# Performance work log

Hardware: AMD Instinct MI355X
Metric: run time of the kernel (lower is better)

Reference implementation:

```python
import jax, jax.numpy as jnp
import numpy as np

DIM, DEPTH, HEADS, DIM_HEAD, MLP = 768, 6, 12, 64, 3072
INNER = HEADS * DIM_HEAD
B, N = 8, 1024
SCALE = DIM_HEAD ** -0.5
EPS = 1e-5


def _ln(x, g, b):
    m = jnp.mean(x, -1, keepdims=True)
    v = jnp.mean(jnp.square(x - m), -1, keepdims=True)
    return (x - m) * jax.lax.rsqrt(v + EPS) * g + b


def _ternary(w):
    # BitNet-style ternary quant with straight-through estimator
    s = jnp.mean(jnp.abs(w)) + 1e-8
    wq = jnp.clip(jnp.round(w / s), -1.0, 1.0) * s
    return w + jax.lax.stop_gradient(wq - w)


def setup_inputs() -> dict:
    key = jax.random.key(0)
    ks = jax.random.split(key, 8)
    d = {
        'x': jax.random.normal(ks[0], (B, N, DIM), jnp.float32),
        'ln1_g': jnp.ones((DEPTH, DIM), jnp.float32),
        'ln1_b': jnp.zeros((DEPTH, DIM), jnp.float32),
        'Wqkv': jax.random.normal(ks[1], (DEPTH, 3 * INNER, DIM), jnp.float32) * 0.02,
        'ln2_g': jnp.ones((DEPTH, INNER), jnp.float32),
        'ln2_b': jnp.zeros((DEPTH, INNER), jnp.float32),
        'Wo': jax.random.normal(ks[2], (DEPTH, DIM, INNER), jnp.float32) * 0.02,
        'bo': jnp.zeros((DEPTH, DIM), jnp.float32),
        'ffln1_g': jnp.ones((DEPTH, DIM), jnp.float32),
        'ffln1_b': jnp.zeros((DEPTH, DIM), jnp.float32),
        'W1': jax.random.normal(ks[3], (DEPTH, MLP, DIM), jnp.float32) * 0.02,
        'b1': jnp.zeros((DEPTH, MLP), jnp.float32),
        'ffln2_g': jnp.ones((DEPTH, MLP), jnp.float32),
        'ffln2_b': jnp.zeros((DEPTH, MLP), jnp.float32),
        'W2': jax.random.normal(ks[4], (DEPTH, DIM, MLP), jnp.float32) * 0.02,
        'b2': jnp.zeros((DEPTH, DIM), jnp.float32),
    }
    return d


def _forward(x, ln1_g, ln1_b, Wqkv, ln2_g, ln2_b, Wo, bo,
             ffln1_g, ffln1_b, W1, b1, ffln2_g, ffln2_b, W2, b2):
    depth = Wqkv.shape[0]
    # layers 0..depth-2 ternary, last layer plain linear
    flag = jnp.concatenate([jnp.ones((depth - 1,), x.dtype), jnp.zeros((1,), x.dtype)])

    def block(h, p):
        (g1, b1n, wqkv, g2, b2n, wo, bo_, fg1, fb1, w1, bb1, fg2, fb2, w2, bb2, f) = p

        def mt(w):
            return f * _ternary(w) + (1.0 - f) * w

        y = _ln(h, g1, b1n)
        qkv = jnp.einsum('bnd,ed->bne', y, mt(wqkv))  # [B,N,3*INNER]
        q, k, v = jnp.split(qkv, 3, axis=-1)
        def heads(t):
            return t.reshape(B, N, HEADS, DIM_HEAD).transpose(0, 2, 1, 3)
        q, k, v = heads(q), heads(k), heads(v)
        attn = jax.nn.softmax(jnp.einsum('bhnd,bhmd->bhnm', q, k) * SCALE, axis=-1)
        o = jnp.einsum('bhnm,bhmd->bhnd', attn, v)
        o = o.transpose(0, 2, 1, 3).reshape(B, N, INNER)
        o = _ln(o, g2, b2n)
        o = jnp.einsum('bne,de->bnd', o, mt(wo)) + bo_
        h = h + o
        y = _ln(h, fg1, fb1)
        y = jnp.einsum('bnd,md->bnm', y, mt(w1)) + bb1
        y = jax.nn.gelu(y, approximate=False)
        y = _ln(y, fg2, fb2)
        y = jnp.einsum('bnm,dm->bnd', y, mt(w2)) + bb2
        return h + y, None

    xs = (ln1_g, ln1_b, Wqkv, ln2_g, ln2_b, Wo, bo,
          ffln1_g, ffln1_b, W1, b1, ffln2_g, ffln2_b, W2, b2, flag)
    out, _ = jax.lax.scan(block, x, xs)
    return out


def reference(x, ln1_g, ln1_b, Wqkv, ln2_g, ln2_b, Wo, bo,
              ffln1_g, ffln1_b, W1, b1, ffln2_g, ffln2_b, W2, b2):
    return _forward(x, ln1_g, ln1_b, Wqkv, ln2_g, ln2_b, Wo, bo,
                    ffln1_g, ffln1_b, W1, b1, ffln2_g, ffln2_b, W2, b2)
```

## Files before the change

kernel.cpp:

```cpp
#include <hip/hip_runtime.h>
#include <hip/hip_bf16.h>
#include <math.h>

typedef __bf16 bf16_t;
typedef __bf16 bf16x4 __attribute__((ext_vector_type(4)));
typedef __bf16 bf16x8 __attribute__((ext_vector_type(8)));
typedef float  f32x4  __attribute__((ext_vector_type(4)));

#define TOKENS 8192
#define DIMV   768
#define INNERV 768
#define QKVW   2304
#define MLPW   3072
#define NSEQ   1024
#define NB     8
#define NH     12
#define DH     64

enum { EP_STORE = 0, EP_BIAS_RES = 1, EP_BIAS_GELU = 2 };

__device__ __forceinline__ void gload_lds16(const bf16_t* g, bf16_t* l)
{
  __builtin_amdgcn_global_load_lds((const __attribute__((address_space(1))) void*)g,
                                   (__attribute__((address_space(3))) void*)l,
                                   16, 0, 0);
}

__device__ __forceinline__ float gelu_fast(float x)
{
  const float z = fabsf(x) * 0.70710678118654752f;
  const float d = fmaf(0.3275911f, z, 1.0f);
  const float t = 1.0f / d;
  float p = fmaf(t, 1.061405429f, -1.453152027f);
  p = fmaf(t, p, 1.421413741f);
  p = fmaf(t, p, -0.284496736f);
  p = fmaf(t, p, 0.254829592f);
  p = t * p;
  const float e = __expf(-z * z);
  float erfv = fmaf(-p, e, 1.0f);
  erfv = copysignf(erfv, x);
  return 0.5f * x * (1.0f + erfv);
}

template <int BM>
__global__ __launch_bounds__(256)
void gemm_nt(const bf16_t* __restrict__ A, const bf16_t* __restrict__ B,
             const int K, const int N, const int mode,
             const float* __restrict__ sacc_p, const float sinvn, const float sbias,
             const float* __restrict__ bias,
             float* __restrict__ resid,
             bf16_t* __restrict__ outb,
             float* __restrict__ fout)
{
  constexpr int MI = BM / 32;
  constexpr int WR = BM / 2;
  __shared__ __align__(16) bf16_t lsAll[3 * BM * 32 + 3 * 128 * 32];
  bf16_t* lsA = lsAll;
  bf16_t* lsB = lsAll + 3 * BM * 32;
  const int tid  = threadIdx.x;
  const int lane = tid & 63;
  const int wave = tid >> 6;
  const int wm = wave >> 1, wn = wave & 1;
  const int bm = blockIdx.x, bn = blockIdx.y;

  const int srB   = wave * 32 + (lane >> 2);
  const int fswB  = (srB >> 1) & 3;
  const int scolB = ((lane & 3) ^ fswB) * 8;
  const bf16_t* gB = B + (size_t)(bn * 128 + srB) * K + scolB;
  const int lb0 = srB * 32 + (lane & 3) * 8;
  const int lb1 = (srB + 16) * 32 + (lane & 3) * 8;

  const int srA   = (BM == 128) ? srB : (wave * 16 + (lane >> 2));
  const int fswA  = (srA >> 1) & 3;
  const int scolA = ((lane & 3) ^ fswA) * 8;
  const bf16_t* gA = A + (size_t)(bm * BM + srA) * K + scolA;
  const int la0 = srA * 32 + (lane & 3) * 8;
  const int la1 = (srA + 16) * 32 + (lane & 3) * 8;

  f32x4 acc[MI][4];
#pragma unroll
  for (int i = 0; i < MI; i++)
#pragma unroll
    for (int j = 0; j < 4; j++) acc[i][j] = (f32x4){0.f, 0.f, 0.f, 0.f};

  const int fr   = ((lane & 15) >> 1) & 3;
  const int rsl  = ((lane >> 4) ^ fr) * 8;
  const int arow = (wm * WR + (lane & 15)) * 32 + rsl;
  const int brow = (wn * 64 + (lane & 15)) * 32 + rsl;

  auto stage = [&](int b, int kb) {
    gload_lds16(gA + kb, &lsA[b * BM * 32 + la0]);
    if constexpr (BM == 128) gload_lds16(gA + (size_t)16 * K + kb, &lsA[b * BM * 32 + la1]);
    gload_lds16(gB + kb, &lsB[b * 128 * 32 + lb0]);
    gload_lds16(gB + (size_t)16 * K + kb, &lsB[b * 128 * 32 + lb1]);
  };
  auto compute = [&](int b) {
    bf16x8 af[MI], bfv[4];
#pragma unroll
    for (int i = 0; i < MI; i++) af[i]  = *(const bf16x8*)&lsA[b * BM * 32 + arow + i * 16 * 32];
#pragma unroll
    for (int j = 0; j < 4; j++)  bfv[j] = *(const bf16x8*)&lsB[b * 128 * 32 + brow + j * 16 * 32];
#pragma unroll
    for (int i = 0; i < MI; i++)
#pragma unroll
      for (int j = 0; j < 4; j++)
        acc[i][j] = __builtin_amdgcn_mfma_f32_16x16x32_bf16(af[i], bfv[j], acc[i][j], 0, 0, 0);
  };

  const int NT = K / 32;
  stage(0, 0);
  stage(1, 32);
  int cb = 0, sb = 2;
  for (int t = 0; t < NT - 1; ++t) {
    if constexpr (BM == 128) asm volatile("s_waitcnt vmcnt(4)" ::: "memory");
    else                     asm volatile("s_waitcnt vmcnt(3)" ::: "memory");
    __builtin_amdgcn_s_barrier();
    __builtin_amdgcn_sched_barrier(0);
    compute(cb);
    if (t + 2 < NT) stage(sb, (t + 2) * 32);
    cb = (cb == 2) ? 0 : cb + 1;
    sb = (sb == 2) ? 0 : sb + 1;
  }
  asm volatile("s_waitcnt vmcnt(0)" ::: "memory");
  __builtin_amdgcn_s_barrier();
  __builtin_amdgcn_sched_barrier(0);
  compute(cb);

  __syncthreads();
  const float s = (*sacc_p) * sinvn + sbias;
  const int lr0 = wm * WR + (lane >> 4) * 4;
  const int lc0 = wn * 64 + (lane & 15);

  if (mode == EP_BIAS_RES) {
    float* ep = (float*)lsAll;
#pragma unroll
    for (int i = 0; i < MI; i++)
#pragma unroll
      for (int j = 0; j < 4; j++) {
        const float bcol = bias[bn * 128 + lc0 + j * 16];
#pragma unroll
        for (int r = 0; r < 4; r++)
          ep[(lr0 + i * 16 + r) * 132 + lc0 + j * 16] = acc[i][j][r] * s + bcol;
      }
    __syncthreads();
#pragma unroll
    for (int it = 0; it < BM / 8; ++it) {
      const int lr = it * 8 + (tid >> 5);
      const int lc = (tid & 31) * 4;
      f32x4 v = *(const f32x4*)&ep[lr * 132 + lc];
      const size_t idx = (size_t)(bm * BM + lr) * N + bn * 128 + lc;
      f32x4 rv = *(const f32x4*)&resid[idx];
      if (fout) *(f32x4*)&fout[idx]  = rv + v;
      else      *(f32x4*)&resid[idx] = rv + v;
    }
  } else {
    bf16_t* ep = lsAll;
#pragma unroll
    for (int i = 0; i < MI; i++)
#pragma unroll
      for (int j = 0; j < 4; j++) {
        const int col = bn * 128 + lc0 + j * 16;
#pragma unroll
        for (int r = 0; r < 4; r++) {
          const float v = acc[i][j][r] * s;
          ep[(lr0 + i * 16 + r) * 136 + lc0 + j * 16] =
              (mode == EP_STORE) ? (bf16_t)v : (bf16_t)gelu_fast(v + bias[col]);
        }
      }
    __syncthreads();
#pragma unroll
    for (int it = 0; it < BM / 16; ++it) {
      const int lr = it * 16 + (tid >> 4);
      const int lc = (tid & 15) * 8;
      bf16x8 v = *(const bf16x8*)&ep[lr * 136 + lc];
      *(bf16x8*)&outb[(size_t)(bm * BM + lr) * N + bn * 128 + lc] = v;
    }
  }
}

template <typename TIN>
__global__ __launch_bounds__(256)
void ln_kern(const TIN* __restrict__ x, const float* __restrict__ g,
             const float* __restrict__ b, bf16_t* __restrict__ y, const int W)
{
  const int row = blockIdx.x;
  const int tid = threadIdx.x;
  const TIN* xr = x + (size_t)row * W;
  float s = 0.f, s2 = 0.f;
  if constexpr (sizeof(TIN) == 4) {
    const f32x4* xv = (const f32x4*)xr;
    for (int i = tid; i < W / 4; i += 256) {
      f32x4 v = xv[i];
#pragma unroll
      for (int e = 0; e < 4; e++) { s += v[e]; s2 += v[e] * v[e]; }
    }
  } else {
    const bf16x8* xv = (const bf16x8*)xr;
    for (int i = tid; i < W / 8; i += 256) {
      bf16x8 v = xv[i];
#pragma unroll
      for (int e = 0; e < 8; e++) { const float f = (float)v[e]; s += f; s2 += f * f; }
    }
  }
#pragma unroll
  for (int off = 32; off > 0; off >>= 1) {
    s  += __shfl_xor(s,  off, 64);
    s2 += __shfl_xor(s2, off, 64);
  }
  __shared__ float red[8];
  if ((tid & 63) == 0) { red[(tid >> 6) * 2] = s; red[(tid >> 6) * 2 + 1] = s2; }
  __syncthreads();
  const float ts  = red[0] + red[2] + red[4] + red[6];
  const float ts2 = red[1] + red[3] + red[5] + red[7];
  const float invW = 1.0f / (float)W;
  const float mean = ts * invW;
  const float var  = fmaxf(ts2 * invW - mean * mean, 0.f);
  const float rs   = rsqrtf(var + 1e-5f);
  bf16_t* yr = y + (size_t)row * W;
  const f32x4* gv = (const f32x4*)g;
  const f32x4* bv = (const f32x4*)b;
  if constexpr (sizeof(TIN) == 4) {
    const f32x4* xv = (const f32x4*)xr;
    bf16x4* yv = (bf16x4*)yr;
    for (int i = tid; i < W / 4; i += 256) {
      f32x4 v = xv[i], gg = gv[i], bb = bv[i];
      bf16x4 o;
#pragma unroll
      for (int e = 0; e < 4; e++) o[e] = (bf16_t)((v[e] - mean) * rs * gg[e] + bb[e]);
      yv[i] = o;
    }
  } else {
    const bf16x8* xv = (const bf16x8*)xr;
    bf16x8* yv = (bf16x8*)yr;
    for (int i = tid; i < W / 8; i += 256) {
      bf16x8 v = xv[i];
      f32x4 g0 = gv[2 * i], g1 = gv[2 * i + 1];
      f32x4 b0 = bv[2 * i], b1 = bv[2 * i + 1];
      bf16x8 o;
#pragma unroll
      for (int e = 0; e < 4; e++) o[e]     = (bf16_t)(((float)v[e]     - mean) * rs * g0[e] + b0[e]);
#pragma unroll
      for (int e = 0; e < 4; e++) o[e + 4] = (bf16_t)(((float)v[e + 4] - mean) * rs * g1[e] + b1[e]);
      yv[i] = o;
    }
  }
}

__global__ __launch_bounds__(256)
void attn_mfma(const bf16_t* __restrict__ qkv, bf16_t* __restrict__ o)
{
  __shared__ __align__(16) bf16_t Ks[64][72];
  __shared__ __align__(16) bf16_t Vt[64][72];
  __shared__ __align__(16) bf16_t Pw[4][16][72];
  const float SCL = 0.125f * 1.44269504088896f;
  const int tid  = threadIdx.x;
  const int lane = tid & 63;
  const int wave = tid >> 6;
  const int quad = lane >> 4;
  const int l15  = lane & 15;
  const int qb = blockIdx.x, hh = blockIdx.y, bb = blockIdx.z;
  const size_t tokbase = (size_t)bb * NSEQ;

  const int qrow = qb * 64 + wave * 16 + l15;
  bf16x8 qf[2];
  {
    const bf16_t* qp = qkv + (tokbase + qrow) * QKVW + hh * DH;
    qf[0] = *(const bf16x8*)(qp + quad * 8);
    qf[1] = *(const bf16x8*)(qp + 32 + quad * 8);
  }

  f32x4 Ot[4];
#pragma unroll
  for (int i = 0; i < 4; i++) Ot[i] = (f32x4){0.f, 0.f, 0.f, 0.f};
  float m2[4], lp[4];
#pragma unroll
  for (int r = 0; r < 4; r++) { m2[r] = -1e30f; lp[r] = 0.f; }

  const int skv = tid & 63;
  const int sd  = (tid >> 6) * 16;

  bf16x8 k0, k1, v0, v1;
  {
    const bf16_t* kp = qkv + (tokbase + skv) * QKVW + INNERV + hh * DH + sd;
    k0 = *(const bf16x8*)kp;
    k1 = *(const bf16x8*)(kp + 8);
    v0 = *(const bf16x8*)(kp + INNERV);
    v1 = *(const bf16x8*)(kp + INNERV + 8);
  }

  for (int kt = 0; kt < NSEQ / 64; ++kt) {
    __syncthreads();
    *(bf16x8*)&Ks[skv][sd]     = k0;
    *(bf16x8*)&Ks[skv][sd + 8] = k1;
#pragma unroll
    for (int e = 0; e < 8; e++) { Vt[sd + e][skv] = v0[e]; Vt[sd + 8 + e][skv] = v1[e]; }
    __syncthreads();

    bf16x8 nk0 = k0, nk1 = k1, nv0 = v0, nv1 = v1;
    if (kt + 1 < NSEQ / 64) {
      const bf16_t* kp = qkv + (tokbase + (kt + 1) * 64 + skv) * QKVW + INNERV + hh * DH + sd;
      nk0 = *(const bf16x8*)kp;
      nk1 = *(const bf16x8*)(kp + 8);
      nv0 = *(const bf16x8*)(kp + INNERV);
      nv1 = *(const bf16x8*)(kp + INNERV + 8);
    }

    f32x4 st[4];
    __builtin_amdgcn_s_setprio(1);
#pragma unroll
    for (int nt = 0; nt < 4; nt++) {
      bf16x8 b0 = *(const bf16x8*)&Ks[nt * 16 + l15][quad * 8];
      bf16x8 b1 = *(const bf16x8*)&Ks[nt * 16 + l15][32 + quad * 8];
      f32x4 c = (f32x4){0.f, 0.f, 0.f, 0.f};
      c = __builtin_amdgcn_mfma_f32_16x16x32_bf16(qf[0], b0, c, 0, 0, 0);
      c = __builtin_amdgcn_mfma_f32_16x16x32_bf16(qf[1], b1, c, 0, 0, 0);
      st[nt] = c;
    }
    __builtin_amdgcn_s_setprio(0);

    float lm[4];
#pragma unroll
    for (int r = 0; r < 4; r++)
      lm[r] = fmaxf(fmaxf(st[0][r], st[1][r]), fmaxf(st[2][r], st[3][r]));
    const bool ok = (lm[0] * SCL <= m2[0] + 8.f) && (lm[1] * SCL <= m2[1] + 8.f) &&
                    (lm[2] * SCL <= m2[2] + 8.f) && (lm[3] * SCL <= m2[3] + 8.f);
    if (!__all(ok)) {
#pragma unroll
      for (int r = 0; r < 4; r++) {
        float v = lm[r];
        v = fmaxf(v, __shfl_xor(v, 1, 64));
        v = fmaxf(v, __shfl_xor(v, 2, 64));
        v = fmaxf(v, __shfl_xor(v, 4, 64));
        v = fmaxf(v, __shfl_xor(v, 8, 64));
        const float rmax2 = v * SCL;
        const float mnew = fmaxf(m2[r], rmax2);
        const float alpha = exp2f(m2[r] - mnew);
        m2[r] = mnew;
        lp[r] *= alpha;
#pragma unroll
        for (int dt = 0; dt < 4; dt++) Ot[dt][r] *= alpha;
      }
    }
#pragma unroll
    for (int nt = 0; nt < 4; nt++) {
#pragma unroll
      for (int r = 0; r < 4; r++) {
        const float p = exp2f(fmaf(st[nt][r], SCL, -m2[r]));
        lp[r] += p;
        Pw[wave][quad * 4 + r][nt * 16 + l15] = (bf16_t)p;
      }
    }

    asm volatile("s_waitcnt lgkmcnt(0)" ::: "memory");
    __builtin_amdgcn_sched_barrier(0);

    __builtin_amdgcn_s_setprio(1);
#pragma unroll
    for (int kk = 0; kk < 2; kk++) {
      bf16x8 pa = *(const bf16x8*)&Pw[wave][l15][kk * 32 + quad * 8];
#pragma unroll
      for (int dt = 0; dt < 4; dt++) {
        bf16x8 vb = *(const bf16x8*)&Vt[dt * 16 + l15][kk * 32 + quad * 8];
        Ot[dt] = __builtin_amdgcn_mfma_f32_16x16x32_bf16(pa, vb, Ot[dt], 0, 0, 0);
      }
    }
    __builtin_amdgcn_s_setprio(0);

    k0 = nk0; k1 = nk1; v0 = nv0; v1 = nv1;
  }

  float inv[4];
#pragma unroll
  for (int r = 0; r < 4; r++) {
    float v = lp[r];
    v += __shfl_xor(v, 1, 64);
    v += __shfl_xor(v, 2, 64);
    v += __shfl_xor(v, 4, 64);
    v += __shfl_xor(v, 8, 64);
    inv[r] = 1.0f / v;
  }
#pragma unroll
  for (int dt = 0; dt < 4; dt++) {
#pragma unroll
    for (int r = 0; r < 4; r++) {
      const int q = qb * 64 + wave * 16 + quad * 4 + r;
      const int d = dt * 16 + l15;
      o[(tokbase + q) * INNERV + hh * DH + d] = (bf16_t)(Ot[dt][r] * inv[r]);
    }
  }
}

__global__ __launch_bounds__(64)
void zero_kern(float* __restrict__ p)
{
  p[threadIdx.x] = 0.f;
}

__global__ __launch_bounds__(256)
void absmean4_kern(const float* __restrict__ w0, const float* __restrict__ w1,
                   const float* __restrict__ w2, const float* __restrict__ w3,
                   const long n0, const long n1, const long n2, const long n3,
                   float* __restrict__ acc)
{
  const int t = blockIdx.y;
  const float* w = (t == 0) ? w0 : (t == 1) ? w1 : (t == 2) ? w2 : w3;
  const long  n  = (t == 0) ? n0 : (t == 1) ? n1 : (t == 2) ? n2 : n3;
  const int tid = threadIdx.x;
  float s = 0.f;
  const size_t stride = (size_t)256 * gridDim.x * 4;
  for (size_t i = ((size_t)blockIdx.x * 256 + tid) * 4; i < (size_t)n; i += stride) {
    f32x4 v = *(const f32x4*)(w + i);
    s += fabsf(v[0]) + fabsf(v[1]) + fabsf(v[2]) + fabsf(v[3]);
  }
#pragma unroll
  for (int off = 32; off > 0; off >>= 1) s += __shfl_xor(s, off, 64);
  __shared__ float red[4];
  if ((tid & 63) == 0) red[tid >> 6] = s;
  __syncthreads();
  if (tid == 0) atomicAdd(&acc[t], red[0] + red[1] + red[2] + red[3]);
}

__global__ __launch_bounds__(256)
void quant4_kern(const float* __restrict__ w0, const float* __restrict__ w1,
                 const float* __restrict__ w2, const float* __restrict__ w3,
                 bf16_t* __restrict__ q0, bf16_t* __restrict__ q1,
                 bf16_t* __restrict__ q2, bf16_t* __restrict__ q3,
                 const int n40, const int n41, const int n42, const int n43,
                 const float* __restrict__ acc,
                 const float inv0, const float inv1, const float inv2, const float inv3)
{
  const int t = blockIdx.y;
  const float* w = (t == 0) ? w0 : (t == 1) ? w1 : (t == 2) ? w2 : w3;
  bf16_t*      q = (t == 0) ? q0 : (t == 1) ? q1 : (t == 2) ? q2 : q3;
  const int   n4 = (t == 0) ? n40 : (t == 1) ? n41 : (t == 2) ? n42 : n43;
  const float iv = (t == 0) ? inv0 : (t == 1) ? inv1 : (t == 2) ? inv2 : inv3;
  const int i = blockIdx.x * 256 + threadIdx.x;
  if (i >= n4) return;
  const float s = acc[t] * iv + 1e-8f;
  f32x4 v = ((const f32x4*)w)[i];
  bf16x4 o;
#pragma unroll
  for (int e = 0; e < 4; e++) {
    float qv = rintf(v[e] / s);
    qv = fminf(1.f, fmaxf(-1.f, qv));
    o[e] = (bf16_t)qv;
  }
  ((bf16x4*)q)[i] = o;
}

__global__ __launch_bounds__(256)
void cast4_kern(const float* __restrict__ w0, const float* __restrict__ w1,
                const float* __restrict__ w2, const float* __restrict__ w3,
                bf16_t* __restrict__ q0, bf16_t* __restrict__ q1,
                bf16_t* __restrict__ q2, bf16_t* __restrict__ q3,
                const int n40, const int n41, const int n42, const int n43)
{
  const int t = blockIdx.y;
  const float* w = (t == 0) ? w0 : (t == 1) ? w1 : (t == 2) ? w2 : w3;
  bf16_t*      q = (t == 0) ? q0 : (t == 1) ? q1 : (t == 2) ? q2 : q3;
  const int   n4 = (t == 0) ? n40 : (t == 1) ? n41 : (t == 2) ? n42 : n43;
  const int i = blockIdx.x * 256 + threadIdx.x;
  if (i >= n4) return;
  f32x4 v = ((const f32x4*)w)[i];
  bf16x4 o;
#pragma unroll
  for (int e = 0; e < 4; e++) o[e] = (bf16_t)v[e];
  ((bf16x4*)q)[i] = o;
}

__global__ __launch_bounds__(256)
void copyf_kern(const float* __restrict__ in, float* __restrict__ out, const int n4)
{
  const int i = blockIdx.x * 256 + threadIdx.x;
  if (i < n4) ((f32x4*)out)[i] = ((const f32x4*)in)[i];
}

extern "C" void kernel_launch(void* const* d_in, const int* in_sizes, int n_in,
                              void* d_out, int out_size, void* d_ws, size_t ws_size,
                              hipStream_t stream)
{
  const float* x     = (const float*)d_in[0];
  const float* ln1_g = (const float*)d_in[1];
  const float* ln1_b = (const float*)d_in[2];
  const float* Wqkv  = (const float*)d_in[3];
  const float* ln2_g = (const float*)d_in[4];
  const float* ln2_b = (const float*)d_in[5];
  const float* Wo    = (const float*)d_in[6];
  const float* bo    = (const float*)d_in[7];
  const float* fg1   = (const float*)d_in[8];
  const float* fb1   = (const float*)d_in[9];
  const float* W1    = (const float*)d_in[10];
  const float* b1    = (const float*)d_in[11];
  const float* fg2   = (const float*)d_in[12];
  const float* fb2   = (const float*)d_in[13];
  const float* W2    = (const float*)d_in[14];
  const float* b2    = (const float*)d_in[15];

  char* ws = (char*)d_ws;
  size_t off = 0;
  float*  sacc  = (float*)(ws + off);  off += 256;
  float*  h     = (float*)(ws + off);  off += (size_t)TOKENS * DIMV * 4;
  bf16_t* bigA  = (bf16_t*)(ws + off); off += (size_t)TOKENS * MLPW * 2;
  bf16_t* bigB  = (bf16_t*)(ws + off); off += (size_t)TOKENS * MLPW * 2;
  bf16_t* q_qkv = (bf16_t*)(ws + off); off += (size_t)QKVW * DIMV * 2;
  bf16_t* q_o   = (bf16_t*)(ws + off); off += (size_t)DIMV * INNERV * 2;
  bf16_t* q_1   = (bf16_t*)(ws + off); off += (size_t)MLPW * DIMV * 2;
  bf16_t* q_2   = (bf16_t*)(ws + off); off += (size_t)DIMV * MLPW * 2;

  bf16_t* obuf   = bigA;
  bf16_t* ln2out = bigA + (size_t)TOKENS * INNERV;

  zero_kern<<<1, 64, 0, stream>>>(sacc);
  copyf_kern<<<TOKENS * DIMV / 4 / 256, 256, 0, stream>>>(x, h, TOKENS * DIMV / 4);

  for (int lyr = 0; lyr < 6; ++lyr) {
    const float* wqkv_l = Wqkv + (size_t)lyr * QKVW * DIMV;
    const float* wo_l   = Wo   + (size_t)lyr * DIMV * INNERV;
    const float* w1_l   = W1   + (size_t)lyr * MLPW * DIMV;
    const float* w2_l   = W2   + (size_t)lyr * DIMV * MLPW;
    const float *sq, *so, *s1, *s2p;
    float iq, io, i1, i2, bq, bo2, bb1v, bb2v;
    if (lyr < 5) {
      absmean4_kern<<<dim3(64, 4), 256, 0, stream>>>(
          wqkv_l, wo_l, w1_l, w2_l,
          (long)QKVW * DIMV, (long)DIMV * INNERV, (long)MLPW * DIMV, (long)DIMV * MLPW,
          &sacc[lyr * 4]);
      quant4_kern<<<dim3(MLPW * DIMV / 1024, 4), 256, 0, stream>>>(
          wqkv_l, wo_l, w1_l, w2_l, q_qkv, q_o, q_1, q_2,
          QKVW * DIMV / 4, DIMV * INNERV / 4, MLPW * DIMV / 4, DIMV * MLPW / 4,
          &sacc[lyr * 4],
          1.0f / (QKVW * DIMV), 1.0f / (DIMV * INNERV), 1.0f / (MLPW * DIMV), 1.0f / (DIMV * MLPW));
      sq = &sacc[lyr * 4 + 0]; iq = 1.0f / (QKVW * DIMV); bq = 1e-8f;
      so = &sacc[lyr * 4 + 1]; io = 1.0f / (DIMV * INNERV); bo2 = 1e-8f;
      s1 = &sacc[lyr * 4 + 2]; i1 = 1.0f / (MLPW * DIMV); bb1v = 1e-8f;
      s2p = &sacc[lyr * 4 + 3]; i2 = 1.0f / (DIMV * MLPW); bb2v = 1e-8f;
    } else {
      cast4_kern<<<dim3(MLPW * DIMV / 1024, 4), 256, 0, stream>>>(
          wqkv_l, wo_l, w1_l, w2_l, q_qkv, q_o, q_1, q_2,
          QKVW * DIMV / 4, DIMV * INNERV / 4, MLPW * DIMV / 4, DIMV * MLPW / 4);
      sq = so = s1 = s2p = &sacc[63];
      iq = io = i1 = i2 = 0.f;
      bq = bo2 = bb1v = bb2v = 1.0f;
    }

    ln_kern<float><<<TOKENS, 256, 0, stream>>>(h, ln1_g + lyr * DIMV, ln1_b + lyr * DIMV, bigA, DIMV);
    gemm_nt<128><<<dim3(64, QKVW / 128), 256, 0, stream>>>(bigA, q_qkv, DIMV, QKVW, EP_STORE, sq, iq, bq, nullptr, nullptr, bigB, nullptr);
    attn_mfma<<<dim3(NSEQ / 64, NH, NB), 256, 0, stream>>>(bigB, obuf);
    ln_kern<bf16_t><<<TOKENS, 256, 0, stream>>>(obuf, ln2_g + lyr * INNERV, ln2_b + lyr * INNERV, ln2out, INNERV);
    gemm_nt<64><<<dim3(TOKENS / 64, DIMV / 128), 256, 0, stream>>>(ln2out, q_o, INNERV, DIMV, EP_BIAS_RES, so, io, bo2, bo + lyr * DIMV, h, nullptr, nullptr);
    ln_kern<float><<<TOKENS, 256, 0, stream>>>(h, fg1 + lyr * DIMV, fb1 + lyr * DIMV, bigA, DIMV);
    gemm_nt<128><<<dim3(64, MLPW / 128), 256, 0, stream>>>(bigA, q_1, DIMV, MLPW, EP_BIAS_GELU, s1, i1, bb1v, b1 + lyr * MLPW, nullptr, bigB, nullptr);
    ln_kern<bf16_t><<<TOKENS, 256, 0, stream>>>(bigB, fg2 + lyr * MLPW, fb2 + lyr * MLPW, bigA, MLPW);
    gemm_nt<64><<<dim3(TOKENS / 64, DIMV / 128), 256, 0, stream>>>(bigA, q_2, MLPW, DIMV, EP_BIAS_RES, s2p, i2, bb2v, b2 + lyr * DIMV, h, nullptr,
                                                                   (lyr == 5) ? (float*)d_out : nullptr);
  }
}
```

Baseline: 2.210 ms.

## Double attention query tile to 128 rows with 512 threads and XCD-aware block order

Each attention block now uses 8 waves covering 128 query rows, so every K/V tile staged in shared memory serves twice as many queries. Per-thread staging load is halved to match. Block IDs are remapped so consecutive blocks spread across the 8 XCDs while blocks of the same head stay grouped for L2 reuse. The absmean reduction grid is also widened. The trade is fewer blocks in flight, and larger blocks may lower occupancy.

```diff
diff --git a/kernel.cpp b/kernel.cpp
--- a/kernel.cpp
+++ b/kernel.cpp
@@ -246,22 +246,28 @@
   }
 }
 
-__global__ __launch_bounds__(256)
+__global__ __launch_bounds__(512)
 void attn_mfma(const bf16_t* __restrict__ qkv, bf16_t* __restrict__ o)
 {
   __shared__ __align__(16) bf16_t Ks[64][72];
   __shared__ __align__(16) bf16_t Vt[64][72];
-  __shared__ __align__(16) bf16_t Pw[4][16][72];
+  __shared__ __align__(16) bf16_t Pw[8][16][72];
   const float SCL = 0.125f * 1.44269504088896f;
   const int tid  = threadIdx.x;
   const int lane = tid & 63;
   const int wave = tid >> 6;
   const int quad = lane >> 4;
   const int l15  = lane & 15;
-  const int qb = blockIdx.x, hh = blockIdx.y, bb = blockIdx.z;
+
+  const int id      = blockIdx.x;
+  const int logical = (id & 7) * 96 + (id >> 3);
+  const int qb   = logical & 7;
+  const int rest = logical >> 3;
+  const int hh   = rest % 12;
+  const int bb   = rest / 12;
   const size_t tokbase = (size_t)bb * NSEQ;
 
-  const int qrow = qb * 64 + wave * 16 + l15;
+  const int qrow = qb * 128 + wave * 16 + l15;
   bf16x8 qf[2];
   {
     const bf16_t* qp = qkv + (tokbase + qrow) * QKVW + hh * DH;
@@ -276,33 +282,28 @@
 #pragma unroll
   for (int r = 0; r < 4; r++) { m2[r] = -1e30f; lp[r] = 0.f; }
 
-  const int skv = tid & 63;
-  const int sd  = (tid >> 6) * 16;
-
-  bf16x8 k0, k1, v0, v1;
+  const int srow = tid & 63;
+  const int sd   = (tid >> 6) * 8;
+
+  bf16x8 k0, v0;
   {
-    const bf16_t* kp = qkv + (tokbase + skv) * QKVW + INNERV + hh * DH + sd;
+    const bf16_t* kp = qkv + (tokbase + srow) * QKVW + INNERV + hh * DH + sd;
     k0 = *(const bf16x8*)kp;
-    k1 = *(const bf16x8*)(kp + 8);
     v0 = *(const bf16x8*)(kp + INNERV);
-    v1 = *(const bf16x8*)(kp + INNERV + 8);
   }
 
   for (int kt = 0; kt < NSEQ / 64; ++kt) {
     __syncthreads();
-    *(bf16x8*)&Ks[skv][sd]     = k0;
-    *(bf16x8*)&Ks[skv][sd + 8] = k1;
-#pragma unroll
-    for (int e = 0; e < 8; e++) { Vt[sd + e][skv] = v0[e]; Vt[sd + 8 + e][skv] = v1[e]; }
+    *(bf16x8*)&Ks[srow][sd] = k0;
+#pragma unroll
+    for (int e = 0; e < 8; e++) Vt[sd + e][srow] = v0[e];
     __syncthreads();
 
-    bf16x8 nk0 = k0, nk1 = k1, nv0 = v0, nv1 = v1;
+    bf16x8 nk0 = k0, nv0 = v0;
     if (kt + 1 < NSEQ / 64) {
-      const bf16_t* kp = qkv + (tokbase + (kt + 1) * 64 + skv) * QKVW + INNERV + hh * DH + sd;
+      const bf16_t* kp = qkv + (tokbase + (kt + 1) * 64 + srow) * QKVW + INNERV + hh * DH + sd;
       nk0 = *(const bf16x8*)kp;
-      nk1 = *(const bf16x8*)(kp + 8);
       nv0 = *(const bf16x8*)(kp + INNERV);
-      nv1 = *(const bf16x8*)(kp + INNERV + 8);
     }
 
     f32x4 st[4];
@@ -366,7 +367,7 @@
     }
     __builtin_amdgcn_s_setprio(0);
 
-    k0 = nk0; k1 = nk1; v0 = nv0; v1 = nv1;
+    k0 = nk0; v0 = nv0;
   }
 
   float inv[4];
@@ -383,7 +384,7 @@
   for (int dt = 0; dt < 4; dt++) {
 #pragma unroll
     for (int r = 0; r < 4; r++) {
-      const int q = qb * 64 + wave * 16 + quad * 4 + r;
+      const int q = qb * 128 + wave * 16 + quad * 4 + r;
       const int d = dt * 16 + l15;
       o[(tokbase + q) * INNERV + hh * DH + d] = (bf16_t)(Ot[dt][r] * inv[r]);
     }
@@ -521,7 +522,7 @@
     const float *sq, *so, *s1, *s2p;
     float iq, io, i1, i2, bq, bo2, bb1v, bb2v;
     if (lyr < 5) {
-      absmean4_kern<<<dim3(64, 4), 256, 0, stream>>>(
+      absmean4_kern<<<dim3(256, 4), 256, 0, stream>>>(
           wqkv_l, wo_l, w1_l, w2_l,
           (long)QKVW * DIMV, (long)DIMV * INNERV, (long)MLPW * DIMV, (long)DIMV * MLPW,
           &sacc[lyr * 4]);
@@ -545,7 +546,7 @@
 
     ln_kern<float><<<TOKENS, 256, 0, stream>>>(h, ln1_g + lyr * DIMV, ln1_b + lyr * DIMV, bigA, DIMV);
     gemm_nt<128><<<dim3(64, QKVW / 128), 256, 0, stream>>>(bigA, q_qkv, DIMV, QKVW, EP_STORE, sq, iq, bq, nullptr, nullptr, bigB, nullptr);
-    attn_mfma<<<dim3(NSEQ / 64, NH, NB), 256, 0, stream>>>(bigB, obuf);
+    attn_mfma<<<NSEQ / 128 * NH * NB, 512, 0, stream>>>(bigB, obuf);
     ln_kern<bf16_t><<<TOKENS, 256, 0, stream>>>(obuf, ln2_g + lyr * INNERV, ln2_b + lyr * INNERV, ln2out, INNERV);
     gemm_nt<64><<<dim3(TOKENS / 64, DIMV / 128), 256, 0, stream>>>(ln2out, q_o, INNERV, DIMV, EP_BIAS_RES, so, io, bo2, bo + lyr * DIMV, h, nullptr, nullptr);
     ln_kern<float><<<TOKENS, 256, 0, stream>>>(h, fg1 + lyr * DIMV, fb1 + lyr * DIMV, bigA, DIMV);
```

Measured after the change: 2.126 ms. 1.04x faster.
